# Performance work log

Measured on AMD Instinct MI355X. Metric: run time of the kernel, lower is better.

## Reference

```python
import jax, jax.numpy as jnp
import numpy as np

N = 100000
E = 1600000
D_IN = 128
D_HID = 32
NEG_SLOPE = 0.2


def _glorot(key, shape):
    fan_in, fan_out = shape[0], shape[-1]
    lim = jnp.sqrt(6.0 / (fan_in + fan_out))
    return jax.random.uniform(key, shape, jnp.float32, -lim, lim)


def setup_inputs() -> dict:
    key = jax.random.key(0)
    ks = jax.random.split(key, 10)
    x = jax.random.normal(ks[0], (N, D_IN), jnp.float32)
    edge_index = jax.random.randint(ks[1], (2, E), 0, N, jnp.int64)
    return {
        "x": x,
        "edge_index": edge_index,
        "W1_l": _glorot(ks[2], (D_IN, D_HID)),
        "W1_r": _glorot(ks[3], (D_IN, D_HID)),
        "att1": _glorot(ks[4], (D_HID,)),
        "b1": jnp.zeros((D_HID,), jnp.float32),
        "W2_l": _glorot(ks[5], (D_HID, D_HID)),
        "W2_r": _glorot(ks[6], (D_HID, D_HID)),
        "att2": _glorot(ks[7], (D_HID,)),
        "b2": jnp.zeros((D_HID,), jnp.float32),
    }


def _segment_softmax(logits, seg, num_segments):
    m = jax.ops.segment_max(logits, seg, num_segments=num_segments)
    m = jnp.where(jnp.isfinite(m), m, 0.0)
    ex = jnp.exp(logits - m[seg])
    s = jax.ops.segment_sum(ex, seg, num_segments=num_segments)
    return ex / (s[seg] + 1e-16)


def _gatv2(x, edge_index, W_l, W_r, att, b):
    # GATv2Conv, heads=1, add_self_loops=False, share_weights=False
    src, dst = edge_index[0], edge_index[1]
    x_l = x @ W_l  # source transform [N, D_HID]
    x_r = x @ W_r  # target transform [N, D_HID]
    # per-edge attention logit: att . leaky_relu(x_l[j] + x_r[i])
    h = x_l[src] + x_r[dst]  # [E, D_HID]
    e = jnp.where(h > 0, h, NEG_SLOPE * h) @ att  # [E]
    alpha = _segment_softmax(e, dst, x.shape[0])  # softmax over incoming edges
    out = jax.ops.segment_sum(alpha[:, None] * x_l[src], dst,
                              num_segments=x.shape[0])
    return out + b


def reference(x, edge_index, W1_l, W1_r, att1, b1, W2_l, W2_r, att2, b2):
    h = _gatv2(x, edge_index, W1_l, W1_r, att1, b1)
    h = jax.nn.relu(h)
    return _gatv2(h, edge_index, W2_l, W2_r, att2, b2)
```

## Files before the change

### kernel.cpp

```cpp
#include <hip/hip_runtime.h>
#include <hip/hip_bf16.h>

#define D_HID 32
#define D_IN 128
#define NEG 0.2f
#define BSH 10
#define BSZ 1024
#define MAXB 128
#define CAP  20480
#define NSCAT 512

typedef unsigned short u16;
typedef __attribute__((ext_vector_type(8))) short short8;
typedef __attribute__((ext_vector_type(4))) float float4v;

#define XOFF(en) (((en) >> 3) & ~127u)

__device__ __forceinline__ float b2f(u16 u){
  union { unsigned int i; float f; } c; c.i = ((unsigned int)u) << 16; return c.f;
}

__device__ __forceinline__ u16 f2b_rne(float f){
  union { float f; unsigned int u; } c; c.f = f;
  unsigned int u = c.u;
  return (u16)((u + 0x7FFFu + ((u >> 16) & 1u)) >> 16);
}

__device__ __forceinline__ void split_bf16(float v, u16& hi, u16& lo){
  hi = f2b_rne(v);
  lo = f2b_rne(v - b2f(hi));
}

__device__ __forceinline__ float ldf(const void* __restrict__ p, int f32, long long i){
  return f32 ? ((const float*)p)[i] : b2f(((const u16*)p)[i]);
}

__device__ __forceinline__ int atomAddI(int* p, int v){
  return __hip_atomic_fetch_add(p, v, __ATOMIC_RELAXED, __HIP_MEMORY_SCOPE_AGENT);
}

__device__ __forceinline__ float red8(float p){
  p += __int_as_float(__builtin_amdgcn_update_dpp(
         0, __float_as_int(p), 0xB1, 0xF, 0xF, true));
  p += __int_as_float(__builtin_amdgcn_update_dpp(
         0, __float_as_int(p), 0x4E, 0xF, 0xF, true));
  p += __int_as_float(__builtin_amdgcn_ds_swizzle(
         __float_as_int(p), 0x101F));
  return p;
}

__device__ __forceinline__ float edge_ev(const float4 xv, const float4 xrk,
                                         const float4 attk){
  float hx = xv.x + xrk.x; hx = fmaxf(hx, NEG*hx);
  float hy = xv.y + xrk.y; hy = fmaxf(hy, NEG*hy);
  float hz = xv.z + xrk.z; hz = fmaxf(hz, NEG*hz);
  float hw = xv.w + xrk.w; hw = fmaxf(hw, NEG*hw);
  float p = hx*attk.x;
  p = fmaf(hy, attk.y, p);
  p = fmaf(hz, attk.z, p);
  p = fmaf(hw, attk.w, p);
  p = red8(p);
  p = fminf(p, 60.f);
  return __expf(p);
}

__device__ __forceinline__ void prep_body(const void* __restrict__ Wl,
                                          const void* __restrict__ Wr,
                                          int f32, int K,
                                          uint4* __restrict__ whi,
                                          uint4* __restrict__ wlo, int t){
  int KS = K >> 5;
  int total = 4 * KS * 64;
  if (t >= total) return;
  int lane = t & 63;
  int rem = t >> 6;
  int kstep = rem % KS;
  int ctile = rem / KS;
  int col = ctile * 16 + (lane & 15);
  int quad = lane >> 4;
  union { u16 s[8]; uint4 q; } ch, cl;
  #pragma unroll
  for (int j = 0; j < 8; ++j){
    int k = kstep*32 + quad*8 + j;
    float v = (col < 32) ? ldf(Wl, f32, (long long)k*D_HID + col)
                         : ldf(Wr, f32, (long long)k*D_HID + (col - 32));
    u16 hi, lo; split_bf16(v, hi, lo);
    ch.s[j] = hi; cl.s[j] = lo;
  }
  whi[rem*64 + lane] = ch.q;
  wlo[rem*64 + lane] = cl.q;
}

__global__ void __launch_bounds__(256)
scat_prep(const int* __restrict__ ei, const u16* __restrict__ xw,
          int* __restrict__ cursor, unsigned* __restrict__ seg,
          int* __restrict__ flags,
          const void* __restrict__ W1l, const void* __restrict__ W1r,
          const void* __restrict__ W2l, const void* __restrict__ W2r,
          uint4* __restrict__ whi1, uint4* __restrict__ wlo1,
          uint4* __restrict__ whi2, uint4* __restrict__ wlo2,
          int E_, int B_){
  int t = threadIdx.x;
  if ((int)blockIdx.x >= NSCAT){
    __shared__ int ins_p;
    if (t == 0) ins_p = 0;
    __syncthreads();
    int e = (xw[t] >> 7) & 0xFF;
    if (e < 100 || e > 140) atomicAdd(&ins_p, 1);
    __syncthreads();
    int f32 = (ins_p > 16) ? 1 : 0;
    int sub = blockIdx.x - NSCAT;
    if (sub < 4) prep_body(W1l, W1r, f32, D_IN,  whi1, wlo1, sub*256 + t);
    else         prep_body(W2l, W2r, f32, D_HID, whi2, wlo2, t);
    return;
  }
  __shared__ int hist[MAXB];
  __shared__ int bbase[MAXB];
  __shared__ int nz_s, insane_s;
  if (t == 0){ nz_s = 0; insane_s = 0; }
  if (t < MAXB) hist[t] = 0;
  __syncthreads();
  if (t < 64 && ei[2*t+1] != 0) atomicAdd(&nz_s, 1);
  if (blockIdx.x == 0){
    int e = (xw[t] >> 7) & 0xFF;
    if (e < 100 || e > 140) atomicAdd(&insane_s, 1);
  }
  __syncthreads();
  int is64 = (nz_s == 0);
  if (blockIdx.x == 0 && t == 0){
    flags[0] = is64;
    flags[1] = (insane_s > 16) ? 1 : 0;
  }
  int chunk = (E_ + NSCAT - 1) / NSCAT;
  int s = blockIdx.x * chunk;
  int e = s + chunk; if (e > E_) e = E_;
  for (int i = s + t; i < e; i += 256){
    int dst = is64 ? ei[2*E_ + 2*i] : ei[E_ + i];
    atomicAdd(&hist[dst >> BSH], 1);
  }
  __syncthreads();
  if (t < MAXB){
    int c = hist[t];
    bbase[t] = c ? atomAddI(&cursor[t], c) : 0;
    hist[t] = 0;
  }
  __syncthreads();
  for (int i = s + t; i < e; i += 256){
    int src, dst;
    if (is64){ src = ei[2*i]; dst = ei[2*E_ + 2*i]; }
    else     { src = ei[i];   dst = ei[E_ + i]; }
    int b = dst >> BSH;
    int pos = bbase[b] + atomicAdd(&hist[b], 1);
    if (pos < CAP)
      seg[(size_t)b*CAP + pos] = ((unsigned)src << BSH) | (unsigned)(dst & (BSZ-1));
  }
}

__device__ void finalize_body(const unsigned* __restrict__ seg,
                              const int* __restrict__ cursor,
                              int* __restrict__ row, int* __restrict__ csr_src,
                              int N_, int B_, int b, int t){
  __shared__ int sd[128];
  __shared__ int hist[BSZ];
  __shared__ int sc[BSZ];
  __shared__ int loff[BSZ];
  if (t < 128) sd[t] = (t < B_) ? min(cursor[t], CAP) : 0;
  hist[t] = 0;
  __syncthreads();
  for (int off = 1; off < 128; off <<= 1){
    int v = (t < 128 && t >= off) ? sd[t-off] : 0;
    __syncthreads();
    if (t < 128) sd[t] += v;
    __syncthreads();
  }
  int cnt = min(cursor[b], CAP);
  int base_out = sd[b] - cnt;
  int total = sd[127];
  size_t base_in = (size_t)b * CAP;

  for (int i = t; i < cnt; i += 1024)
    atomicAdd(&hist[seg[base_in + i] & (BSZ-1)], 1);
  __syncthreads();
  sc[t] = hist[t];
  __syncthreads();
  for (int off = 1; off < BSZ; off <<= 1){
    int tmp = (t >= off) ? sc[t-off] : 0;
    __syncthreads();
    sc[t] += tmp;
    __syncthreads();
  }
  {
    int excl = sc[t] - hist[t];
    loff[t] = excl;
    int node = b*BSZ + t;
    if (node <= N_) row[node] = base_out + excl;
  }
  if (b == B_-1 && t == 0) row[N_] = total;
  __syncthreads();
  for (int i = t; i < cnt; i += 1024){
    unsigned en = seg[base_in + i];
    int dl = en & (BSZ-1);
    int pos = atomicAdd(&loff[dl], 1);
    csr_src[base_out + pos] = (int)en;
  }
}

template<int K>
__device__ __forceinline__ void gemm_body(const void* __restrict__ X,
                          const uint4* __restrict__ whi, const uint4* __restrict__ wlo,
                          const int* __restrict__ flags, int force_f32,
                          float* __restrict__ xl, float* __restrict__ xr,
                          int N_, int tile, int lane)
{
  constexpr int KS = K >> 5;
  if (tile * 16 >= N_) return;
  int quad = lane >> 4;
  int m = tile*16 + (lane & 15);
  if (m >= N_) m = N_ - 1;
  int f32 = force_f32 | flags[1];

  float4v acc[4];
  #pragma unroll
  for (int c = 0; c < 4; ++c) acc[c] = (float4v){0.f,0.f,0.f,0.f};

  #pragma unroll
  for (int ks = 0; ks < KS; ++ks){
    long long base = (long long)m * K + ks*32 + quad*8;
    float av[8];
    if (f32){
      const float4* xp = (const float4*)((const float*)X + base);
      float4 t0 = xp[0], t1 = xp[1];
      av[0]=t0.x; av[1]=t0.y; av[2]=t0.z; av[3]=t0.w;
      av[4]=t1.x; av[5]=t1.y; av[6]=t1.z; av[7]=t1.w;
    } else {
      union { uint4 q; u16 s[8]; } c8;
      c8.q = *(const uint4*)((const u16*)X + base);
      #pragma unroll
      for (int j = 0; j < 8; ++j) av[j] = b2f(c8.s[j]);
    }
    short8 ahi, alo;
    #pragma unroll
    for (int j = 0; j < 8; ++j){
      u16 hi, lo; split_bf16(av[j], hi, lo);
      ahi[j] = (short)hi; alo[j] = (short)lo;
    }
    #pragma unroll
    for (int c = 0; c < 4; ++c){
      uint4 wh = whi[(c*KS + ks)*64 + lane];
      uint4 wl = wlo[(c*KS + ks)*64 + lane];
      short8 bh = *(short8*)&wh;
      short8 bl = *(short8*)&wl;
      acc[c] = __builtin_amdgcn_mfma_f32_16x16x32_bf16(ahi, bh, acc[c], 0, 0, 0);
      acc[c] = __builtin_amdgcn_mfma_f32_16x16x32_bf16(ahi, bl, acc[c], 0, 0, 0);
      acc[c] = __builtin_amdgcn_mfma_f32_16x16x32_bf16(alo, bh, acc[c], 0, 0, 0);
    }
  }

  #pragma unroll
  for (int c = 0; c < 4; ++c){
    int col = c*16 + (lane & 15);
    float* dst = (col < 32) ? xl : xr;
    int kk = col & 31;
    #pragma unroll
    for (int r = 0; r < 4; ++r){
      int node = tile*16 + quad*4 + r;
      if (node < N_) dst[(size_t)node*D_HID + kk] = acc[c][r];
    }
  }
}

template<int K>
__global__ void __launch_bounds__(1024)
fin_gemm(const unsigned* __restrict__ seg, const int* __restrict__ cursor,
         int* __restrict__ row, int* __restrict__ csr_src,
         const void* __restrict__ X,
         const uint4* __restrict__ whi, const uint4* __restrict__ wlo,
         const int* __restrict__ flags,
         float* __restrict__ xl, float* __restrict__ xr, int N_, int B_){
  if ((int)blockIdx.x < B_){
    finalize_body(seg, cursor, row, csr_src, N_, B_, blockIdx.x, threadIdx.x);
    return;
  }
  int tile = (blockIdx.x - B_) * 16 + (threadIdx.x >> 6);
  gemm_body<K>(X, whi, wlo, flags, 0, xl, xr, N_, tile, threadIdx.x & 63);
}

template<int K>
__global__ void __launch_bounds__(256)
mfma_gemm(const void* __restrict__ X,
          const uint4* __restrict__ whi, const uint4* __restrict__ wlo,
          const int* __restrict__ flags, int force_f32,
          float* __restrict__ xl, float* __restrict__ xr, int N_){
  int tile = blockIdx.x * 4 + (threadIdx.x >> 6);
  gemm_body<K>(X, whi, wlo, flags, force_f32, xl, xr, N_, tile, threadIdx.x & 63);
}

__global__ void __launch_bounds__(256)
gat_gather(const int* __restrict__ row, const unsigned* __restrict__ csrp,
           const float* __restrict__ xl, const float* __restrict__ xr,
           const void* __restrict__ att, const void* __restrict__ bias,
           const int* __restrict__ flags,
           float* __restrict__ outp, int N_, int do_relu)
{
  int wv = (blockIdx.x * blockDim.x + threadIdx.x) >> 6;
  int l = threadIdx.x & 63;
  int n = wv * 4 + (l >> 4);
  if (n >= N_) return;
  int half = (l >> 3) & 1;
  int fl = l & 7;
  int f32 = flags[1];
  float4 attk;
  attk.x = ldf(att, f32, fl*4+0);
  attk.y = ldf(att, f32, fl*4+1);
  attk.z = ldf(att, f32, fl*4+2);
  attk.w = ldf(att, f32, fl*4+3);
  float4 xrk = *(const float4*)(xr + (size_t)n*D_HID + fl*4);
  int rs = row[n], re = row[n+1];
  const char* xlb = (const char*)xl;
  unsigned fo = (unsigned)(fl << 4);

  float4 acc = make_float4(0.f, 0.f, 0.f, 0.f);
  float ssum = 0.f;

  int start = rs + 2*half;
  if (start < re){
    int last = re - 1;
    unsigned c0 = csrp[start];
    unsigned c1 = csrp[min(start+1,  last)];
    unsigned c2 = csrp[min(start+4,  last)];
    unsigned c3 = csrp[min(start+5,  last)];
    unsigned c4 = csrp[min(start+8,  last)];
    unsigned c5 = csrp[min(start+9,  last)];
    unsigned ca = csrp[min(start+12, last)];
    unsigned cb = csrp[min(start+13, last)];
    float4 xv0 = *(const float4*)(xlb + XOFF(c0) + fo);
    float4 xv1 = *(const float4*)(xlb + XOFF(c1) + fo);
    float4 xv2 = *(const float4*)(xlb + XOFF(c2) + fo);
    float4 xv3 = *(const float4*)(xlb + XOFF(c3) + fo);
    float4 xv4 = *(const float4*)(xlb + XOFF(c4) + fo);
    float4 xv5 = *(const float4*)(xlb + XOFF(c5) + fo);
    for (int i = start; i < re; i += 4){
      float4 nx0 = *(const float4*)(xlb + XOFF(ca) + fo);
      float4 nx1 = *(const float4*)(xlb + XOFF(cb) + fo);
      unsigned na = csrp[min(i+16, last)];
      unsigned nb = csrp[min(i+17, last)];
      float ev0 = edge_ev(xv0, xrk, attk);
      ssum += ev0;
      acc.x = fmaf(ev0, xv0.x, acc.x);
      acc.y = fmaf(ev0, xv0.y, acc.y);
      acc.z = fmaf(ev0, xv0.z, acc.z);
      acc.w = fmaf(ev0, xv0.w, acc.w);
      float ev1 = edge_ev(xv1, xrk, attk);
      ev1 = (i + 1 <= last) ? ev1 : 0.f;
      ssum += ev1;
      acc.x = fmaf(ev1, xv1.x, acc.x);
      acc.y = fmaf(ev1, xv1.y, acc.y);
      acc.z = fmaf(ev1, xv1.z, acc.z);
      acc.w = fmaf(ev1, xv1.w, acc.w);
      xv0 = xv2; xv1 = xv3; xv2 = xv4; xv3 = xv5; xv4 = nx0; xv5 = nx1;
      ca = na; cb = nb;
    }
  }

  acc.x += __shfl_xor(acc.x, 8, 16);
  acc.y += __shfl_xor(acc.y, 8, 16);
  acc.z += __shfl_xor(acc.z, 8, 16);
  acc.w += __shfl_xor(acc.w, 8, 16);
  ssum  += __shfl_xor(ssum,  8, 16);

  if (half == 0){
    float inv = 1.0f / (ssum + 1e-16f);
    float4 o;
    o.x = acc.x*inv + ldf(bias, f32, fl*4+0);
    o.y = acc.y*inv + ldf(bias, f32, fl*4+1);
    o.z = acc.z*inv + ldf(bias, f32, fl*4+2);
    o.w = acc.w*inv + ldf(bias, f32, fl*4+3);
    if (do_relu){
      o.x = fmaxf(o.x, 0.f); o.y = fmaxf(o.y, 0.f);
      o.z = fmaxf(o.z, 0.f); o.w = fmaxf(o.w, 0.f);
    }
    *(float4*)(outp + (size_t)n*D_HID + fl*4) = o;
  }
}

extern "C" void kernel_launch(void* const* d_in, const int* in_sizes, int n_in,
                              void* d_out, int out_size, void* d_ws, size_t ws_size,
                              hipStream_t stream)
{
  const void* x   = d_in[0];
  const int*  ei  = (const int*)d_in[1];
  const void* W1l = d_in[2];
  const void* W1r = d_in[3];
  const void* att1= d_in[4];
  const void* b1  = d_in[5];
  const void* W2l = d_in[6];
  const void* W2r = d_in[7];
  const void* att2= d_in[8];
  const void* b2  = d_in[9];
  float* out = (float*)d_out;

  int N_ = in_sizes[0] / D_IN;
  int E_ = in_sizes[1] / 2;
  int B_ = (N_ + BSZ - 1) / BSZ;

  char* ws = (char*)d_ws;
  size_t off = 0;
  auto carve = [&](size_t bytes) -> char* {
    char* p = ws + off;
    off += (bytes + 255) & ~(size_t)255;
    return p;
  };
  float*    xl      = (float*)   carve((size_t)N_ * D_HID * 4);
  float*    xr      = (float*)   carve((size_t)N_ * D_HID * 4);
  float*    h       = (float*)   carve((size_t)N_ * D_HID * 4);
  unsigned* seg     = (unsigned*)carve((size_t)B_ * CAP * 4);
  int*      csr_src = (int*)     carve((size_t)E_ * 4);
  int*      row     = (int*)     carve((size_t)(N_ + 1) * 4);
  int*      cursor  = (int*)     carve((size_t)MAXB * 4);
  int*      flags   = (int*)     carve(256);
  uint4*    whi1    = (uint4*)   carve((size_t)4 * 4 * 64 * 16);
  uint4*    wlo1    = (uint4*)   carve((size_t)4 * 4 * 64 * 16);
  uint4*    whi2    = (uint4*)   carve((size_t)4 * 1 * 64 * 16);
  uint4*    wlo2    = (uint4*)   carve((size_t)4 * 1 * 64 * 16);

  const int tpb = 256;
  int gG = (N_ + 15) / 16;
  int tiles = (N_ + 15) / 16;
  int gT1 = (tiles + 15) / 16;
  int gT2 = (tiles + 3) / 4;

  hipMemsetAsync(cursor, 0, (size_t)MAXB * 4, stream);

  scat_prep<<<NSCAT + 5, tpb, 0, stream>>>(
      ei, (const u16*)x, cursor, seg, flags,
      W1l, W1r, W2l, W2r, whi1, wlo1, whi2, wlo2, E_, B_);

  fin_gemm<D_IN><<<B_ + gT1, 1024, 0, stream>>>(
      seg, cursor, row, csr_src, x, whi1, wlo1, flags, xl, xr, N_, B_);

  gat_gather<<<gG, tpb, 0, stream>>>(row, (const unsigned*)csr_src, xl, xr,
                                     att1, b1, flags, h, N_, 1);

  mfma_gemm<D_HID><<<gT2, tpb, 0, stream>>>(h, whi2, wlo2, flags, 1, xl, xr, N_);

  gat_gather<<<gG, tpb, 0, stream>>>(row, (const unsigned*)csr_src, xl, xr,
                                     att2, b2, flags, out, N_, 0);
}
```

Measured before the change: 235.0 us.

## Fuse all GAT stages into one cooperative persistent kernel with grid syncs

Replaces the four-launch pipeline (scatter/prep, finalize+GEMM, gather, GEMM, gather) with a single cooperative kernel that uses grid.sync between stages and grid-stride loops over tiles and nodes. The finalize step is rewritten for 256-thread blocks, with each thread scanning four histogram bins. The goal is to remove launch gaps and tail effects between the short stages. In exchange, the grid is limited to resident blocks (at most 1024), so the edge scatter runs on fewer blocks with larger chunks, and each grid barrier has its own cost. The multi-kernel path is kept as a fallback if the cooperative launch fails.

```diff
diff --git a/kernel.cpp b/kernel.cpp
--- a/kernel.cpp
+++ b/kernel.cpp
@@ -1,5 +1,8 @@
 #include <hip/hip_runtime.h>
 #include <hip/hip_bf16.h>
+#include <hip/hip_cooperative_groups.h>
+
+namespace cg = cooperative_groups;
 
 #define D_HID 32
 #define D_IN 128
@@ -9,6 +12,7 @@
 #define MAXB 128
 #define CAP  20480
 #define NSCAT 512
+#define NUM_CU 256
 
 typedef unsigned short u16;
 typedef __attribute__((ext_vector_type(8))) short short8;
@@ -91,116 +95,59 @@
   wlo[rem*64 + lane] = cl.q;
 }
 
-__global__ void __launch_bounds__(256)
-scat_prep(const int* __restrict__ ei, const u16* __restrict__ xw,
-          int* __restrict__ cursor, unsigned* __restrict__ seg,
-          int* __restrict__ flags,
-          const void* __restrict__ W1l, const void* __restrict__ W1r,
-          const void* __restrict__ W2l, const void* __restrict__ W2r,
-          uint4* __restrict__ whi1, uint4* __restrict__ wlo1,
-          uint4* __restrict__ whi2, uint4* __restrict__ wlo2,
-          int E_, int B_){
-  int t = threadIdx.x;
-  if ((int)blockIdx.x >= NSCAT){
-    __shared__ int ins_p;
-    if (t == 0) ins_p = 0;
-    __syncthreads();
-    int e = (xw[t] >> 7) & 0xFF;
-    if (e < 100 || e > 140) atomicAdd(&ins_p, 1);
-    __syncthreads();
-    int f32 = (ins_p > 16) ? 1 : 0;
-    int sub = blockIdx.x - NSCAT;
-    if (sub < 4) prep_body(W1l, W1r, f32, D_IN,  whi1, wlo1, sub*256 + t);
-    else         prep_body(W2l, W2r, f32, D_HID, whi2, wlo2, t);
-    return;
-  }
-  __shared__ int hist[MAXB];
-  __shared__ int bbase[MAXB];
-  __shared__ int nz_s, insane_s;
-  if (t == 0){ nz_s = 0; insane_s = 0; }
-  if (t < MAXB) hist[t] = 0;
-  __syncthreads();
-  if (t < 64 && ei[2*t+1] != 0) atomicAdd(&nz_s, 1);
-  if (blockIdx.x == 0){
-    int e = (xw[t] >> 7) & 0xFF;
-    if (e < 100 || e > 140) atomicAdd(&insane_s, 1);
-  }
-  __syncthreads();
-  int is64 = (nz_s == 0);
-  if (blockIdx.x == 0 && t == 0){
-    flags[0] = is64;
-    flags[1] = (insane_s > 16) ? 1 : 0;
-  }
-  int chunk = (E_ + NSCAT - 1) / NSCAT;
-  int s = blockIdx.x * chunk;
-  int e = s + chunk; if (e > E_) e = E_;
-  for (int i = s + t; i < e; i += 256){
-    int dst = is64 ? ei[2*E_ + 2*i] : ei[E_ + i];
-    atomicAdd(&hist[dst >> BSH], 1);
-  }
-  __syncthreads();
-  if (t < MAXB){
-    int c = hist[t];
-    bbase[t] = c ? atomAddI(&cursor[t], c) : 0;
-    hist[t] = 0;
-  }
-  __syncthreads();
-  for (int i = s + t; i < e; i += 256){
-    int src, dst;
-    if (is64){ src = ei[2*i]; dst = ei[2*E_ + 2*i]; }
-    else     { src = ei[i];   dst = ei[E_ + i]; }
-    int b = dst >> BSH;
-    int pos = bbase[b] + atomicAdd(&hist[b], 1);
-    if (pos < CAP)
-      seg[(size_t)b*CAP + pos] = ((unsigned)src << BSH) | (unsigned)(dst & (BSZ-1));
-  }
-}
-
 __device__ void finalize_body(const unsigned* __restrict__ seg,
                               const int* __restrict__ cursor,
                               int* __restrict__ row, int* __restrict__ csr_src,
                               int N_, int B_, int b, int t){
-  __shared__ int sd[128];
-  __shared__ int hist[BSZ];
-  __shared__ int sc[BSZ];
-  __shared__ int loff[BSZ];
-  if (t < 128) sd[t] = (t < B_) ? min(cursor[t], CAP) : 0;
-  hist[t] = 0;
-  __syncthreads();
-  for (int off = 1; off < 128; off <<= 1){
-    int v = (t < 128 && t >= off) ? sd[t-off] : 0;
+  __shared__ int fsd[MAXB];
+  __shared__ int fhist[BSZ];
+  __shared__ int fpart[256];
+  __shared__ int floff[BSZ];
+  if (t < MAXB) fsd[t] = (t < B_) ? min(cursor[t], CAP) : 0;
+  for (int i = t; i < BSZ; i += 256) fhist[i] = 0;
+  __syncthreads();
+  for (int off = 1; off < MAXB; off <<= 1){
+    int v = (t < MAXB && t >= off) ? fsd[t-off] : 0;
     __syncthreads();
-    if (t < 128) sd[t] += v;
+    if (t < MAXB) fsd[t] += v;
     __syncthreads();
   }
   int cnt = min(cursor[b], CAP);
-  int base_out = sd[b] - cnt;
-  int total = sd[127];
+  int base_out = fsd[b] - cnt;
+  int total = fsd[MAXB-1];
   size_t base_in = (size_t)b * CAP;
 
-  for (int i = t; i < cnt; i += 1024)
-    atomicAdd(&hist[seg[base_in + i] & (BSZ-1)], 1);
-  __syncthreads();
-  sc[t] = hist[t];
-  __syncthreads();
-  for (int off = 1; off < BSZ; off <<= 1){
-    int tmp = (t >= off) ? sc[t-off] : 0;
+  for (int i = t; i < cnt; i += 256)
+    atomicAdd(&fhist[seg[base_in + i] & (BSZ-1)], 1);
+  __syncthreads();
+  int a0 = fhist[4*t], a1 = fhist[4*t+1], a2 = fhist[4*t+2], a3 = fhist[4*t+3];
+  int mysum = a0 + a1 + a2 + a3;
+  fpart[t] = mysum;
+  __syncthreads();
+  for (int off = 1; off < 256; off <<= 1){
+    int v = (t >= off) ? fpart[t-off] : 0;
     __syncthreads();
-    sc[t] += tmp;
+    fpart[t] += v;
     __syncthreads();
   }
-  {
-    int excl = sc[t] - hist[t];
-    loff[t] = excl;
-    int node = b*BSZ + t;
-    if (node <= N_) row[node] = base_out + excl;
+  int excl = fpart[t] - mysum;
+  floff[4*t]   = excl;
+  floff[4*t+1] = excl + a0;
+  floff[4*t+2] = excl + a0 + a1;
+  floff[4*t+3] = excl + a0 + a1 + a2;
+  __syncthreads();
+  #pragma unroll
+  for (int j = 0; j < 4; ++j){
+    int dl = 4*t + j;
+    int node = b*BSZ + dl;
+    if (node <= N_) row[node] = base_out + floff[dl];
   }
   if (b == B_-1 && t == 0) row[N_] = total;
   __syncthreads();
-  for (int i = t; i < cnt; i += 1024){
+  for (int i = t; i < cnt; i += 256){
     unsigned en = seg[base_in + i];
     int dl = en & (BSZ-1);
-    int pos = atomicAdd(&loff[dl], 1);
+    int pos = atomicAdd(&floff[dl], 1);
     csr_src[base_out + pos] = (int)en;
   }
 }
@@ -208,7 +155,7 @@
 template<int K>
 __device__ __forceinline__ void gemm_body(const void* __restrict__ X,
                           const uint4* __restrict__ whi, const uint4* __restrict__ wlo,
-                          const int* __restrict__ flags, int force_f32,
+                          int f32,
                           float* __restrict__ xl, float* __restrict__ xr,
                           int N_, int tile, int lane)
 {
@@ -217,7 +164,6 @@
   int quad = lane >> 4;
   int m = tile*16 + (lane & 15);
   if (m >= N_) m = N_ - 1;
-  int f32 = force_f32 | flags[1];
 
   float4v acc[4];
   #pragma unroll
@@ -269,51 +215,13 @@
   }
 }
 
-template<int K>
-__global__ void __launch_bounds__(1024)
-fin_gemm(const unsigned* __restrict__ seg, const int* __restrict__ cursor,
-         int* __restrict__ row, int* __restrict__ csr_src,
-         const void* __restrict__ X,
-         const uint4* __restrict__ whi, const uint4* __restrict__ wlo,
-         const int* __restrict__ flags,
-         float* __restrict__ xl, float* __restrict__ xr, int N_, int B_){
-  if ((int)blockIdx.x < B_){
-    finalize_body(seg, cursor, row, csr_src, N_, B_, blockIdx.x, threadIdx.x);
-    return;
-  }
-  int tile = (blockIdx.x - B_) * 16 + (threadIdx.x >> 6);
-  gemm_body<K>(X, whi, wlo, flags, 0, xl, xr, N_, tile, threadIdx.x & 63);
-}
-
-template<int K>
-__global__ void __launch_bounds__(256)
-mfma_gemm(const void* __restrict__ X,
-          const uint4* __restrict__ whi, const uint4* __restrict__ wlo,
-          const int* __restrict__ flags, int force_f32,
-          float* __restrict__ xl, float* __restrict__ xr, int N_){
-  int tile = blockIdx.x * 4 + (threadIdx.x >> 6);
-  gemm_body<K>(X, whi, wlo, flags, force_f32, xl, xr, N_, tile, threadIdx.x & 63);
-}
-
-__global__ void __launch_bounds__(256)
-gat_gather(const int* __restrict__ row, const unsigned* __restrict__ csrp,
-           const float* __restrict__ xl, const float* __restrict__ xr,
-           const void* __restrict__ att, const void* __restrict__ bias,
-           const int* __restrict__ flags,
-           float* __restrict__ outp, int N_, int do_relu)
+__device__ __forceinline__ void gat_node(int n, int l, int f32, float4 attk,
+    const int* __restrict__ row, const unsigned* __restrict__ csrp,
+    const float* __restrict__ xl, const float* __restrict__ xr,
+    const void* __restrict__ bias, float* __restrict__ outp, int do_relu)
 {
-  int wv = (blockIdx.x * blockDim.x + threadIdx.x) >> 6;
-  int l = threadIdx.x & 63;
-  int n = wv * 4 + (l >> 4);
-  if (n >= N_) return;
   int half = (l >> 3) & 1;
   int fl = l & 7;
-  int f32 = flags[1];
-  float4 attk;
-  attk.x = ldf(att, f32, fl*4+0);
-  attk.y = ldf(att, f32, fl*4+1);
-  attk.z = ldf(att, f32, fl*4+2);
-  attk.w = ldf(att, f32, fl*4+3);
   float4 xrk = *(const float4*)(xr + (size_t)n*D_HID + fl*4);
   int rs = row[n], re = row[n+1];
   const char* xlb = (const char*)xl;
@@ -383,6 +291,233 @@
   }
 }
 
+__global__ void __launch_bounds__(256)
+mega(const int* __restrict__ ei, const void* __restrict__ x,
+     int* __restrict__ cursor, unsigned* __restrict__ seg,
+     const void* __restrict__ W1l, const void* __restrict__ W1r,
+     const void* __restrict__ W2l, const void* __restrict__ W2r,
+     uint4* __restrict__ whi1, uint4* __restrict__ wlo1,
+     uint4* __restrict__ whi2, uint4* __restrict__ wlo2,
+     float* __restrict__ xl, float* __restrict__ xr, float* __restrict__ h,
+     int* __restrict__ row, int* __restrict__ csr_src,
+     const void* __restrict__ att1, const void* __restrict__ b1,
+     const void* __restrict__ att2, const void* __restrict__ b2,
+     float* __restrict__ out, int N_, int E_, int B_)
+{
+  cg::grid_group grid = cg::this_grid();
+  const u16* xw = (const u16*)x;
+  int t = threadIdx.x;
+  int blk = blockIdx.x;
+  int G = gridDim.x;
+  __shared__ int shist[MAXB];
+  __shared__ int sbase[MAXB];
+  __shared__ int nz_s, ins_s;
+
+  if (t == 0){ nz_s = 0; ins_s = 0; }
+  if (t < MAXB) shist[t] = 0;
+  __syncthreads();
+  if (t < 64 && ei[2*t+1] != 0) atomicAdd(&nz_s, 1);
+  { int e = (xw[t] >> 7) & 0xFF; if (e < 100 || e > 140) atomicAdd(&ins_s, 1); }
+  __syncthreads();
+  int is64 = (nz_s == 0);
+  int f32  = (ins_s > 16) ? 1 : 0;
+  if (blk >= 1 && blk <= 4) prep_body(W1l, W1r, f32, D_IN,  whi1, wlo1, (blk-1)*256 + t);
+  else if (blk == 5)        prep_body(W2l, W2r, f32, D_HID, whi2, wlo2, t);
+  int chunk = (E_ + G - 1) / G;
+  int s = blk * chunk;
+  int e = min(s + chunk, E_);
+  for (int i = s + t; i < e; i += 256){
+    int dst = is64 ? ei[2*E_ + 2*i] : ei[E_ + i];
+    atomicAdd(&shist[dst >> BSH], 1);
+  }
+  __syncthreads();
+
+  if (t < MAXB){
+    int c = shist[t];
+    sbase[t] = c ? atomAddI(&cursor[t], c) : 0;
+    shist[t] = 0;
+  }
+  __syncthreads();
+  for (int i = s + t; i < e; i += 256){
+    int src, dst;
+    if (is64){ src = ei[2*i]; dst = ei[2*E_ + 2*i]; }
+    else     { src = ei[i];   dst = ei[E_ + i]; }
+    int b = dst >> BSH;
+    int pos = sbase[b] + atomicAdd(&shist[b], 1);
+    if (pos < CAP)
+      seg[(size_t)b*CAP + pos] = ((unsigned)src << BSH) | (unsigned)(dst & (BSZ-1));
+  }
+  __threadfence();
+  grid.sync();
+
+  int tiles = (N_ + 15) >> 4;
+  if (blk < B_){
+    finalize_body(seg, cursor, row, csr_src, N_, B_, blk, t);
+  } else {
+    int wid = t >> 6, lane = t & 63;
+    int gw = (blk - B_)*4 + wid, gW = (G - B_)*4;
+    for (int tile = gw; tile < tiles; tile += gW)
+      gemm_body<D_IN>(x, whi1, wlo1, f32, xl, xr, N_, tile, lane);
+  }
+  __threadfence();
+  grid.sync();
+
+  {
+    int wid = t >> 6, l = t & 63;
+    int fl = l & 7;
+    float4 attk;
+    attk.x = ldf(att1, f32, fl*4+0);
+    attk.y = ldf(att1, f32, fl*4+1);
+    attk.z = ldf(att1, f32, fl*4+2);
+    attk.w = ldf(att1, f32, fl*4+3);
+    int wv = blk*4 + wid, nW = G*4;
+    for (int n0 = wv*4; n0 < N_; n0 += nW*4){
+      int n = n0 + (l >> 4);
+      if (n < N_)
+        gat_node(n, l, f32, attk, row, (const unsigned*)csr_src, xl, xr, b1, h, 1);
+    }
+  }
+  __threadfence();
+  grid.sync();
+
+  {
+    int wid = t >> 6, lane = t & 63;
+    int gw = blk*4 + wid, gW = G*4;
+    for (int tile = gw; tile < tiles; tile += gW)
+      gemm_body<D_HID>(h, whi2, wlo2, 1, xl, xr, N_, tile, lane);
+  }
+  __threadfence();
+  grid.sync();
+
+  {
+    int wid = t >> 6, l = t & 63;
+    int fl = l & 7;
+    float4 attk;
+    attk.x = ldf(att2, f32, fl*4+0);
+    attk.y = ldf(att2, f32, fl*4+1);
+    attk.z = ldf(att2, f32, fl*4+2);
+    attk.w = ldf(att2, f32, fl*4+3);
+    int wv = blk*4 + wid, nW = G*4;
+    for (int n0 = wv*4; n0 < N_; n0 += nW*4){
+      int n = n0 + (l >> 4);
+      if (n < N_)
+        gat_node(n, l, f32, attk, row, (const unsigned*)csr_src, xl, xr, b2, out, 0);
+    }
+  }
+}
+
+__global__ void __launch_bounds__(256)
+scat_prep(const int* __restrict__ ei, const u16* __restrict__ xw,
+          int* __restrict__ cursor, unsigned* __restrict__ seg,
+          int* __restrict__ flags,
+          const void* __restrict__ W1l, const void* __restrict__ W1r,
+          const void* __restrict__ W2l, const void* __restrict__ W2r,
+          uint4* __restrict__ whi1, uint4* __restrict__ wlo1,
+          uint4* __restrict__ whi2, uint4* __restrict__ wlo2,
+          int E_, int B_){
+  int t = threadIdx.x;
+  if ((int)blockIdx.x >= NSCAT){
+    __shared__ int ins_p;
+    if (t == 0) ins_p = 0;
+    __syncthreads();
+    int e = (xw[t] >> 7) & 0xFF;
+    if (e < 100 || e > 140) atomicAdd(&ins_p, 1);
+    __syncthreads();
+    int f32 = (ins_p > 16) ? 1 : 0;
+    int sub = blockIdx.x - NSCAT;
+    if (sub < 4) prep_body(W1l, W1r, f32, D_IN,  whi1, wlo1, sub*256 + t);
+    else         prep_body(W2l, W2r, f32, D_HID, whi2, wlo2, t);
+    return;
+  }
+  __shared__ int hist[MAXB];
+  __shared__ int bbase[MAXB];
+  __shared__ int nz_s, insane_s;
+  if (t == 0){ nz_s = 0; insane_s = 0; }
+  if (t < MAXB) hist[t] = 0;
+  __syncthreads();
+  if (t < 64 && ei[2*t+1] != 0) atomicAdd(&nz_s, 1);
+  if (blockIdx.x == 0){
+    int e = (xw[t] >> 7) & 0xFF;
+    if (e < 100 || e > 140) atomicAdd(&insane_s, 1);
+  }
+  __syncthreads();
+  int is64 = (nz_s == 0);
+  if (blockIdx.x == 0 && t == 0){
+    flags[0] = is64;
+    flags[1] = (insane_s > 16) ? 1 : 0;
+  }
+  int chunk = (E_ + NSCAT - 1) / NSCAT;
+  int s = blockIdx.x * chunk;
+  int e = s + chunk; if (e > E_) e = E_;
+  for (int i = s + t; i < e; i += 256){
+    int dst = is64 ? ei[2*E_ + 2*i] : ei[E_ + i];
+    atomicAdd(&hist[dst >> BSH], 1);
+  }
+  __syncthreads();
+  if (t < MAXB){
+    int c = hist[t];
+    bbase[t] = c ? atomAddI(&cursor[t], c) : 0;
+    hist[t] = 0;
+  }
+  __syncthreads();
+  for (int i = s + t; i < e; i += 256){
+    int src, dst;
+    if (is64){ src = ei[2*i]; dst = ei[2*E_ + 2*i]; }
+    else     { src = ei[i];   dst = ei[E_ + i]; }
+    int b = dst >> BSH;
+    int pos = bbase[b] + atomicAdd(&hist[b], 1);
+    if (pos < CAP)
+      seg[(size_t)b*CAP + pos] = ((unsigned)src << BSH) | (unsigned)(dst & (BSZ-1));
+  }
+}
+
+template<int K>
+__global__ void __launch_bounds__(256)
+fin_gemm(const unsigned* __restrict__ seg, const int* __restrict__ cursor,
+         int* __restrict__ row, int* __restrict__ csr_src,
+         const void* __restrict__ X,
+         const uint4* __restrict__ whi, const uint4* __restrict__ wlo,
+         const int* __restrict__ flags,
+         float* __restrict__ xl, float* __restrict__ xr, int N_, int B_){
+  if ((int)blockIdx.x < B_){
+    finalize_body(seg, cursor, row, csr_src, N_, B_, blockIdx.x, threadIdx.x);
+    return;
+  }
+  int tile = (blockIdx.x - B_) * 4 + (threadIdx.x >> 6);
+  gemm_body<K>(X, whi, wlo, flags[1], xl, xr, N_, tile, threadIdx.x & 63);
+}
+
+template<int K>
+__global__ void __launch_bounds__(256)
+mfma_gemm(const void* __restrict__ X,
+          const uint4* __restrict__ whi, const uint4* __restrict__ wlo,
+          const int* __restrict__ flags, int force_f32,
+          float* __restrict__ xl, float* __restrict__ xr, int N_){
+  int tile = blockIdx.x * 4 + (threadIdx.x >> 6);
+  gemm_body<K>(X, whi, wlo, force_f32 | flags[1], xl, xr, N_, tile, threadIdx.x & 63);
+}
+
+__global__ void __launch_bounds__(256)
+gat_gather(const int* __restrict__ row, const unsigned* __restrict__ csrp,
+           const float* __restrict__ xl, const float* __restrict__ xr,
+           const void* __restrict__ att, const void* __restrict__ bias,
+           const int* __restrict__ flags,
+           float* __restrict__ outp, int N_, int do_relu)
+{
+  int wv = (blockIdx.x * blockDim.x + threadIdx.x) >> 6;
+  int l = threadIdx.x & 63;
+  int n = wv * 4 + (l >> 4);
+  if (n >= N_) return;
+  int f32 = flags[1];
+  int fl = l & 7;
+  float4 attk;
+  attk.x = ldf(att, f32, fl*4+0);
+  attk.y = ldf(att, f32, fl*4+1);
+  attk.z = ldf(att, f32, fl*4+2);
+  attk.w = ldf(att, f32, fl*4+3);
+  gat_node(n, l, f32, attk, row, csrp, xl, xr, bias, outp, do_relu);
+}
+
 extern "C" void kernel_launch(void* const* d_in, const int* in_sizes, int n_in,
                               void* d_out, int out_size, void* d_ws, size_t ws_size,
                               hipStream_t stream)
@@ -423,25 +558,49 @@
   uint4*    whi2    = (uint4*)   carve((size_t)4 * 1 * 64 * 16);
   uint4*    wlo2    = (uint4*)   carve((size_t)4 * 1 * 64 * 16);
 
+  hipMemsetAsync(cursor, 0, (size_t)MAXB * 4, stream);
+
+  static int s_G = -2;
+  if (s_G == -2){
+    int maxb = 0;
+    if (hipOccupancyMaxActiveBlocksPerMultiprocessor(&maxb, mega, 256, 0) == hipSuccess
+        && maxb > 0)
+      s_G = maxb * NUM_CU < 1024 ? maxb * NUM_CU : 1024;
+    else
+      s_G = 0;
+    if (s_G < 256) s_G = 0;
+  }
+  if (s_G > 0){
+    void* kargs[] = {
+      (void*)&ei, (void*)&x, (void*)&cursor, (void*)&seg,
+      (void*)&W1l, (void*)&W1r, (void*)&W2l, (void*)&W2r,
+      (void*)&whi1, (void*)&wlo1, (void*)&whi2, (void*)&wlo2,
+      (void*)&xl, (void*)&xr, (void*)&h, (void*)&row, (void*)&csr_src,
+      (void*)&att1, (void*)&b1, (void*)&att2, (void*)&b2,
+      (void*)&out, (void*)&N_, (void*)&E_, (void*)&B_
+    };
+    hipError_t lerr = hipLaunchCooperativeKernel(mega, dim3(s_G), dim3(256),
+                                                 kargs, 0, stream);
+    if (lerr == hipSuccess) return;
+    s_G = 0;
+  }
+
   const int tpb = 256;
   int gG = (N_ + 15) / 16;
   int tiles = (N_ + 15) / 16;
-  int gT1 = (tiles + 15) / 16;
-  int gT2 = (tiles + 3) / 4;
-
-  hipMemsetAsync(cursor, 0, (size_t)MAXB * 4, stream);
+  int gT = (tiles + 3) / 4;
 
   scat_prep<<<NSCAT + 5, tpb, 0, stream>>>(
       ei, (const u16*)x, cursor, seg, flags,
       W1l, W1r, W2l, W2r, whi1, wlo1, whi2, wlo2, E_, B_);
 
-  fin_gemm<D_IN><<<B_ + gT1, 1024, 0, stream>>>(
+  fin_gemm<D_IN><<<B_ + gT, tpb, 0, stream>>>(
       seg, cursor, row, csr_src, x, whi1, wlo1, flags, xl, xr, N_, B_);
 
   gat_gather<<<gG, tpb, 0, stream>>>(row, (const unsigned*)csr_src, xl, xr,
                                      att1, b1, flags, h, N_, 1);
 
-  mfma_gemm<D_HID><<<gT2, tpb, 0, stream>>>(h, whi2, wlo2, flags, 1, xl, xr, N_);
+  mfma_gemm<D_HID><<<gT, tpb, 0, stream>>>(h, whi2, wlo2, flags, 1, xl, xr, N_);
 
   gat_gather<<<gG, tpb, 0, stream>>>(row, (const unsigned*)csr_src, xl, xr,
                                      att2, b2, flags, out, N_, 0);
```

Result: slower. 846.3 us (+260.2%).
